# Kernel optimization log

Measured on AMD Instinct MI355X. Metric: run time of the kernel, lower is better.

Reference implementation:

```python
import jax, jax.numpy as jnp
import numpy as np

B, N, K, H = 4, 2048, 48, 128
EDGE = 128
FF = 4 * H
SCALE = 30.0


def setup_inputs() -> dict:
    key = jax.random.key(0)
    ks = jax.random.split(key, 12)
    s = lambda fan_in: 1.0 / np.sqrt(fan_in)
    return {
        "h_V": jax.random.normal(ks[0], (B, N, H), jnp.float32),
        "h_E": jax.random.normal(ks[1], (B, N, K, EDGE), jnp.float32),
        "E_idx": jax.random.randint(ks[2], (B, N, K), 0, N, jnp.int32),
        "mask_V": jnp.ones((B, N), jnp.float32),
        "mask_attend": jnp.ones((B, N, K), jnp.float32),
        "W1_w": jax.random.normal(ks[3], (H + EDGE, H), jnp.float32) * s(H + EDGE),
        "W1_b": jnp.zeros((H,), jnp.float32),
        "W2_w": jax.random.normal(ks[4], (H, H), jnp.float32) * s(H),
        "W2_b": jnp.zeros((H,), jnp.float32),
        "W3_w": jax.random.normal(ks[5], (H, H), jnp.float32) * s(H),
        "W3_b": jnp.zeros((H,), jnp.float32),
        "Win_w": jax.random.normal(ks[6], (H, FF), jnp.float32) * s(H),
        "Win_b": jnp.zeros((FF,), jnp.float32),
        "Wout_w": jax.random.normal(ks[7], (FF, H), jnp.float32) * s(FF),
        "Wout_b": jnp.zeros((H,), jnp.float32),
    }


def reference(h_V, h_E, E_idx, mask_V, mask_attend,
              W1_w, W1_b, W2_w, W2_b, W3_w, W3_b,
              Win_w, Win_b, Wout_w, Wout_b):
    gelu_tanh = lambda x: jax.nn.gelu(x, approximate=True)   # self.act = jax.nn.gelu (default approx)
    gelu_exact = lambda x: jax.nn.gelu(x, approximate=False)  # FFN uses approximate=False

    # gather neighbor node features: [B,N,K,H]
    h_nb = jax.vmap(lambda hv, idx: hv[idx])(h_V, E_idx)
    h_EV = jnp.concatenate([h_nb, h_E], axis=-1)              # [B,N,K,H+EDGE]

    # 3-layer message MLP
    m = gelu_tanh(jnp.einsum('bnkc,ch->bnkh', h_EV, W1_w) + W1_b)
    m = gelu_tanh(jnp.einsum('bnkh,hg->bnkg', m, W2_w) + W2_b)
    m = jnp.einsum('bnkg,gh->bnkh', m, W3_w) + W3_b

    m = mask_attend[..., None] * m
    dh = jnp.sum(m, axis=-2) / SCALE                          # [B,N,H]
    h = h_V + dh                                              # dropout rate 0 (eval)

    # position-wise FFN
    ff = gelu_exact(jnp.einsum('bnh,hf->bnf', h, Win_w) + Win_b)
    dh2 = jnp.einsum('bnf,fh->bnh', ff, Wout_w) + Wout_b
    h = h + dh2

    return mask_V[..., None] * h
```

## Files before the change

kernel.cpp:

```cpp
#include <hip/hip_runtime.h>
#include <hip/hip_bf16.h>
#include <math.h>

typedef __attribute__((ext_vector_type(8))) short bf16x8;
typedef __attribute__((ext_vector_type(4))) float f32x4;

#define MFMA16(a,b,c) __builtin_amdgcn_mfma_f32_16x16x32_bf16((a),(b),(c),0,0,0)

union U8 { uint4 u; bf16x8 v; };

__device__ __forceinline__ unsigned int pack2(float a, float b){
  __hip_bfloat162 h = __float22bfloat162_rn(float2{a, b});
  union { __hip_bfloat162 h; unsigned int u; } v; v.h = h;
  return v.u;
}
__device__ __forceinline__ float bflo(unsigned int u){ union{unsigned int i; float f;} v; v.i = u << 16; return v.f; }
__device__ __forceinline__ float bfhi(unsigned int u){ union{unsigned int i; float f;} v; v.i = u & 0xffff0000u; return v.f; }

__device__ __forceinline__ float gelu_tanh_f(float x){
  float x2 = x * x;
  float z  = x * fmaf(x2, -0.10294823f, -2.3022082f);
  float e  = exp2f(z);
  return x * __builtin_amdgcn_rcpf(1.0f + e);
}
__device__ __forceinline__ float gelu_erf_f(float x){
  return 0.5f * x * (1.0f + erff(x * 0.70710678118654752f));
}

__global__ void k_prep(const float* __restrict__ W1, const float* __restrict__ W2,
                       const float* __restrict__ W3, const float* __restrict__ Win,
                       const float* __restrict__ Wout, unsigned short* __restrict__ wt)
{
  int t = blockIdx.x * 256 + threadIdx.x;
  if (t >= 196608) return;
  float v;
  if (t < 32768){            int o = t >> 8,        i = t & 255;         v = W1[i*128 + o]; }
  else if (t < 49152){       int l = t - 32768, o = l >> 7, i = l & 127; v = W2[i*128 + o]; }
  else if (t < 65536){       int l = t - 49152, o = l >> 7, i = l & 127; v = W3[i*128 + o]; }
  else if (t < 131072){      int l = t - 65536, o = l >> 7, i = l & 127; v = Win[i*512 + o]; }
  else {                     int l = t - 131072, o = l >> 9, i = l & 511; v = Wout[i*128 + o]; }
  union { float f; unsigned int u; } w; w.f = v;
  unsigned int r = w.u + 0x7fffu + ((w.u >> 16) & 1u);
  wt[t] = (unsigned short)(r >> 16);
}

__global__ __launch_bounds__(256)
void k_hvp(const float* __restrict__ hV, const unsigned short* __restrict__ wt,
           const float* __restrict__ b1, unsigned short* __restrict__ hVpb)
{
  __shared__ char sH[32*256];
  const int tid = threadIdx.x;
  const int wv  = tid >> 6;
  const int ln  = tid & 63;
  const int l15 = ln & 15;
  const int l4  = ln >> 4;
  const int swz = (l15 & 7) << 4;
  const unsigned short* W1T = wt;
  const int nb = blockIdx.x * 32;

#pragma unroll
  for (int it = 0; it < 2; ++it){
    int cid = tid + it*256;
    int r = cid >> 4, cb = cid & 15;
    const float* src = hV + (size_t)(nb + r)*128 + cb*8;
    float4 a0 = *(const float4*)(src);
    float4 a1 = *(const float4*)(src + 4);
    uint4 w;
    w.x = pack2(a0.x, a0.y); w.y = pack2(a0.z, a0.w);
    w.z = pack2(a1.x, a1.y); w.w = pack2(a1.z, a1.w);
    *(uint4*)(&sH[r*256 + ((cb*16) ^ ((r&7)<<4))]) = w;
  }
  __syncthreads();

  f32x4 acc[2][2];
#pragma unroll
  for (int m = 0; m < 2; ++m){ acc[m][0] = f32x4{0.f,0.f,0.f,0.f}; acc[m][1] = f32x4{0.f,0.f,0.f,0.f}; }
#pragma unroll
  for (int ks = 0; ks < 4; ++ks){
    bf16x8 x0 = *(const bf16x8*)(&sH[(l15)*256      + ((ks*64 + l4*16) ^ swz)]);
    bf16x8 x1 = *(const bf16x8*)(&sH[(16 + l15)*256 + ((ks*64 + l4*16) ^ swz)]);
#pragma unroll
    for (int m = 0; m < 2; ++m){
      int orow = (wv*2 + m)*16 + l15;
      bf16x8 wf = *(const bf16x8*)(W1T + orow*256 + ks*32 + l4*8);
      acc[m][0] = MFMA16(wf, x0, acc[m][0]);
      acc[m][1] = MFMA16(wf, x1, acc[m][1]);
    }
  }
#pragma unroll
  for (int m = 0; m < 2; ++m){
    int och0 = (wv*2 + m)*16 + l4*4;
    float q0 = b1[och0], q1 = b1[och0+1], q2 = b1[och0+2], q3 = b1[och0+3];
#pragma unroll
    for (int nt = 0; nt < 2; ++nt){
      int node = nb + nt*16 + l15;
      uint2 p;
      p.x = pack2(acc[m][nt][0] + q0, acc[m][nt][1] + q1);
      p.y = pack2(acc[m][nt][2] + q2, acc[m][nt][3] + q3);
      *(uint2*)(hVpb + (size_t)node*128 + och0) = p;
    }
  }
}

__global__ __launch_bounds__(256, 2)
void k_msg(const float* __restrict__ hE, const int* __restrict__ Eidx,
           const float* __restrict__ maskA, const unsigned short* __restrict__ wt,
           const unsigned short* __restrict__ hVpb, const float* __restrict__ b2,
           float* __restrict__ S, float* __restrict__ msums)
{
  __shared__ char sW1[32768];

  const int tid = threadIdx.x;
  const int wv  = tid >> 6;
  const int ln  = tid & 63;
  const int l15 = ln & 15;
  const int l4  = ln >> 4;
  const int wswz = (l15 & 7) << 4;

  const unsigned short* W2G = wt + 32768;

#pragma unroll
  for (int it = 0; it < 8; ++it){
    int f = tid + it*256;
    int r = f >> 4, cb = f & 15;
    uint4 w1c = *(const uint4*)(wt + r*256 + 128 + cb*8);
    *(uint4*)(&sW1[r*256 + ((cb*16) ^ ((r&7)<<4))]) = w1c;
  }
  __syncthreads();

  const int node = blockIdx.x * 4 + wv;
  const size_t bb = ((size_t)(node >> 11)) << 11;

  int eidx0, eidx1, eidx2; float emk0, emk1, emk2;
  {
    const int*   ip = Eidx  + node*48 + l15;
    const float* mp = maskA + node*48 + l15;
    eidx0 = ip[0]; eidx1 = ip[16]; eidx2 = ip[32];
    emk0  = mp[0]; emk1  = mp[16]; emk2  = mp[32];
  }

  f32x4 ssum[8];
#pragma unroll
  for (int t = 0; t < 8; ++t) ssum[t] = f32x4{0.f,0.f,0.f,0.f};

#pragma unroll
  for (int c = 0; c < 3; ++c){
    const int   cidx = (c == 0) ? eidx0 : (c == 1) ? eidx1 : eidx2;
    const float cmk  = (c == 0) ? emk0  : (c == 1) ? emk1  : emk2;

    const float* xp = hE + (size_t)(node*48 + c*16 + l15)*128 + l4*8;
    float4 xr[8];
#pragma unroll
    for (int ks = 0; ks < 4; ++ks){
      xr[2*ks]   = *(const float4*)(xp + ks*32);
      xr[2*ks+1] = *(const float4*)(xp + ks*32 + 4);
    }
    uint2 hp[8];
    {
      const unsigned short* hb = hVpb + (bb + (size_t)cidx)*128 + l4*4;
#pragma unroll
      for (int t = 0; t < 8; ++t) hp[t] = *(const uint2*)(hb + 16*t);
    }
    bf16x8 xf[4];
#pragma unroll
    for (int ks = 0; ks < 4; ++ks){
      U8 xu;
      xu.u.x = pack2(xr[2*ks].x,   xr[2*ks].y);
      xu.u.y = pack2(xr[2*ks].z,   xr[2*ks].w);
      xu.u.z = pack2(xr[2*ks+1].x, xr[2*ks+1].y);
      xu.u.w = pack2(xr[2*ks+1].z, xr[2*ks+1].w);
      xf[ks] = xu.v;
    }

    f32x4 a1[8];
#pragma unroll
    for (int t = 0; t < 8; ++t) a1[t] = f32x4{0.f,0.f,0.f,0.f};
#pragma unroll
    for (int ks = 0; ks < 4; ++ks){
#pragma unroll
      for (int t = 0; t < 8; ++t){
        bf16x8 wf = *(const bf16x8*)(&sW1[(16*t + l15)*256 + ((ks*64 + l4*16) ^ wswz)]);
        a1[t] = MFMA16(wf, xf[ks], a1[t]);
      }
    }

    unsigned int q[8][2];
#pragma unroll
    for (int t = 0; t < 8; ++t){
      float g0 = gelu_tanh_f(a1[t][0] + bflo(hp[t].x));
      float g1 = gelu_tanh_f(a1[t][1] + bfhi(hp[t].x));
      float g2 = gelu_tanh_f(a1[t][2] + bflo(hp[t].y));
      float g3 = gelu_tanh_f(a1[t][3] + bfhi(hp[t].y));
      q[t][0] = pack2(g0, g1);
      q[t][1] = pack2(g2, g3);
    }

    f32x4 a2[8];
#pragma unroll
    for (int t = 0; t < 8; ++t) a2[t] = f32x4{0.f,0.f,0.f,0.f};
    const bool lo = (l4 < 2);
    const int srcbase = l15 + 32*(l4 & 1);
#pragma unroll
    for (int ks2 = 0; ks2 < 4; ++ks2){
      unsigned int xw[4];
#pragma unroll
      for (int p = 0; p < 4; ++p){
        int src = srcbase + 16*(p >> 1);
        unsigned int va = (unsigned int)__shfl((int)q[2*ks2][p & 1],     src, 64);
        unsigned int vb = (unsigned int)__shfl((int)q[2*ks2 + 1][p & 1], src, 64);
        xw[p] = lo ? va : vb;
      }
      U8 xb; xb.u.x = xw[0]; xb.u.y = xw[1]; xb.u.z = xw[2]; xb.u.w = xw[3];
#pragma unroll
      for (int t = 0; t < 8; ++t){
        bf16x8 wf = *(const bf16x8*)(W2G + (16*t + l15)*128 + ks2*32 + l4*8);
        a2[t] = MFMA16(wf, xb.v, a2[t]);
      }
    }

#pragma unroll
    for (int t = 0; t < 8; ++t){
      const float4 bq = *(const float4*)(b2 + 16*t + l4*4);
      ssum[t][0] += cmk * gelu_tanh_f(a2[t][0] + bq.x);
      ssum[t][1] += cmk * gelu_tanh_f(a2[t][1] + bq.y);
      ssum[t][2] += cmk * gelu_tanh_f(a2[t][2] + bq.z);
      ssum[t][3] += cmk * gelu_tanh_f(a2[t][3] + bq.w);
    }
  }

#pragma unroll
  for (int t = 0; t < 8; ++t){
#pragma unroll
    for (int r = 0; r < 4; ++r){
#pragma unroll
      for (int off = 1; off < 16; off <<= 1)
        ssum[t][r] += __shfl_xor(ssum[t][r], off, 16);
    }
  }
  if (l15 == 0){
#pragma unroll
    for (int t = 0; t < 8; ++t){
      float4 o;
      o.x = ssum[t][0] * (1.0f/30.0f);
      o.y = ssum[t][1] * (1.0f/30.0f);
      o.z = ssum[t][2] * (1.0f/30.0f);
      o.w = ssum[t][3] * (1.0f/30.0f);
      *(float4*)(S + (size_t)node*128 + 16*t + l4*4) = o;
    }
  }
  {
    float qs = emk0 + emk1 + emk2;
#pragma unroll
    for (int off = 1; off < 16; off <<= 1) qs += __shfl_xor(qs, off, 16);
    if (ln == 0) msums[node] = qs * (1.0f/30.0f);
  }
}

__global__ __launch_bounds__(256, 2)
void k_ffn(const float* __restrict__ hV, const float* __restrict__ S,
           const float* __restrict__ msums, const float* __restrict__ maskV,
           const unsigned short* __restrict__ wt,
           const float* __restrict__ b3, const float* __restrict__ bin,
           const float* __restrict__ bout, float* __restrict__ out)
{
  __shared__ char  sS[32*256];
  __shared__ char  sH[32*256];
  __shared__ float sHf[32*132];
  __shared__ char  sF[32*1024];

  const int tid = threadIdx.x;
  const int wv  = tid >> 6;
  const int ln  = tid & 63;
  const int l15 = ln & 15;
  const int l4  = ln >> 4;
  const int swz = (l15 & 7) << 4;
  const unsigned short* W3T   = wt + 49152;
  const unsigned short* WinT  = wt + 65536;
  const unsigned short* WoutT = wt + 131072;
  const int nb = blockIdx.x * 32;

#pragma unroll
  for (int it = 0; it < 2; ++it){
    int cid = tid + it*256;
    int r = cid >> 4, cb = cid & 15;
    const float* src = S + (size_t)(nb + r)*128 + cb*8;
    float4 a0 = *(const float4*)(src);
    float4 a1 = *(const float4*)(src + 4);
    uint4 w;
    w.x = pack2(a0.x, a0.y); w.y = pack2(a0.z, a0.w);
    w.z = pack2(a1.x, a1.y); w.w = pack2(a1.z, a1.w);
    *(uint4*)(&sS[r*256 + ((cb*16) ^ ((r&7)<<4))]) = w;
  }
  __syncthreads();

  {
    f32x4 acc[2][2];
#pragma unroll
    for (int m = 0; m < 2; ++m){ acc[m][0] = f32x4{0.f,0.f,0.f,0.f}; acc[m][1] = f32x4{0.f,0.f,0.f,0.f}; }
#pragma unroll
    for (int ks = 0; ks < 4; ++ks){
      bf16x8 x0 = *(const bf16x8*)(&sS[(l15)*256      + ((ks*64 + l4*16) ^ swz)]);
      bf16x8 x1 = *(const bf16x8*)(&sS[(16 + l15)*256 + ((ks*64 + l4*16) ^ swz)]);
#pragma unroll
      for (int m = 0; m < 2; ++m){
        int cr = (wv*2 + m)*16 + l15;
        bf16x8 wf = *(const bf16x8*)(W3T + cr*128 + ks*32 + l4*8);
        acc[m][0] = MFMA16(wf, x0, acc[m][0]);
        acc[m][1] = MFMA16(wf, x1, acc[m][1]);
      }
    }
#pragma unroll
    for (int m = 0; m < 2; ++m){
      int ch0 = (wv*2 + m)*16 + l4*4;
      const float4 b3q = *(const float4*)(b3 + ch0);
#pragma unroll
      for (int nt = 0; nt < 2; ++nt){
        int row  = nt*16 + l15;
        int node = nb + row;
        float ms = msums[node];
        const float4 hv = *(const float4*)(hV + (size_t)node*128 + ch0);
        float h0 = hv.x + acc[m][nt][0] + ms*b3q.x;
        float h1 = hv.y + acc[m][nt][1] + ms*b3q.y;
        float h2 = hv.z + acc[m][nt][2] + ms*b3q.z;
        float h3 = hv.w + acc[m][nt][3] + ms*b3q.w;
        float4 hf; hf.x = h0; hf.y = h1; hf.z = h2; hf.w = h3;
        *(float4*)(&sHf[row*132 + ch0]) = hf;
        uint2 p; p.x = pack2(h0, h1); p.y = pack2(h2, h3);
        *(uint2*)(&sH[row*256 + ((ch0*2) ^ ((row&7)<<4))]) = p;
      }
    }
  }
  __syncthreads();

  f32x4 accA[8][2];
#pragma unroll
  for (int m8 = 0; m8 < 8; ++m8){ accA[m8][0] = f32x4{0.f,0.f,0.f,0.f}; accA[m8][1] = f32x4{0.f,0.f,0.f,0.f}; }
#pragma unroll
  for (int ks = 0; ks < 4; ++ks){
    bf16x8 x0 = *(const bf16x8*)(&sH[(l15)*256      + ((ks*64 + l4*16) ^ swz)]);
    bf16x8 x1 = *(const bf16x8*)(&sH[(16 + l15)*256 + ((ks*64 + l4*16) ^ swz)]);
#pragma unroll
    for (int m8 = 0; m8 < 8; ++m8){
      int fr = (wv*8 + m8)*16 + l15;
      bf16x8 wf = *(const bf16x8*)(WinT + fr*128 + ks*32 + l4*8);
      accA[m8][0] = MFMA16(wf, x0, accA[m8][0]);
      accA[m8][1] = MFMA16(wf, x1, accA[m8][1]);
    }
  }
#pragma unroll
  for (int m8 = 0; m8 < 8; ++m8){
    int f0 = (wv*8 + m8)*16 + l4*4;
    float q0 = bin[f0], q1 = bin[f0+1], q2 = bin[f0+2], q3 = bin[f0+3];
#pragma unroll
    for (int nt = 0; nt < 2; ++nt){
      int row = nt*16 + l15;
      float g0 = gelu_erf_f(accA[m8][nt][0] + q0);
      float g1 = gelu_erf_f(accA[m8][nt][1] + q1);
      float g2 = gelu_erf_f(accA[m8][nt][2] + q2);
      float g3 = gelu_erf_f(accA[m8][nt][3] + q3);
      uint2 p; p.x = pack2(g0, g1); p.y = pack2(g2, g3);
      *(uint2*)(&sF[row*1024 + ((f0*2) ^ swz)]) = p;
    }
  }
  __syncthreads();

  f32x4 accB[2][2];
#pragma unroll
  for (int m = 0; m < 2; ++m){ accB[m][0] = f32x4{0.f,0.f,0.f,0.f}; accB[m][1] = f32x4{0.f,0.f,0.f,0.f}; }
#pragma unroll
  for (int ks = 0; ks < 16; ++ks){
    bf16x8 x0 = *(const bf16x8*)(&sF[(l15)*1024      + ((ks*64 + l4*16) ^ swz)]);
    bf16x8 x1 = *(const bf16x8*)(&sF[(16 + l15)*1024 + ((ks*64 + l4*16) ^ swz)]);
#pragma unroll
    for (int m = 0; m < 2; ++m){
      int cr = (wv*2 + m)*16 + l15;
      bf16x8 wf = *(const bf16x8*)(WoutT + cr*512 + ks*32 + l4*8);
      accB[m][0] = MFMA16(wf, x0, accB[m][0]);
      accB[m][1] = MFMA16(wf, x1, accB[m][1]);
    }
  }
#pragma unroll
  for (int m = 0; m < 2; ++m){
    int ch0 = (wv*2 + m)*16 + l4*4;
    float q0 = bout[ch0], q1 = bout[ch0+1], q2 = bout[ch0+2], q3 = bout[ch0+3];
#pragma unroll
    for (int nt = 0; nt < 2; ++nt){
      int row  = nt*16 + l15;
      int node = nb + row;
      float mv = maskV[node];
      const float4 hf = *(const float4*)(&sHf[row*132 + ch0]);
      float4 o;
      o.x = mv * (hf.x + accB[m][nt][0] + q0);
      o.y = mv * (hf.y + accB[m][nt][1] + q1);
      o.z = mv * (hf.z + accB[m][nt][2] + q2);
      o.w = mv * (hf.w + accB[m][nt][3] + q3);
      *(float4*)(out + (size_t)node*128 + ch0) = o;
    }
  }
}

extern "C" void kernel_launch(void* const* d_in, const int* in_sizes, int n_in,
                              void* d_out, int out_size, void* d_ws, size_t ws_size,
                              hipStream_t stream)
{
  const float* hV    = (const float*)d_in[0];
  const float* hE    = (const float*)d_in[1];
  const int*   Eidx  = (const int*)  d_in[2];
  const float* maskV = (const float*)d_in[3];
  const float* maskA = (const float*)d_in[4];
  const float* W1w = (const float*)d_in[5];
  const float* W1b = (const float*)d_in[6];
  const float* W2w = (const float*)d_in[7];
  const float* W2b = (const float*)d_in[8];
  const float* W3w = (const float*)d_in[9];
  const float* W3b = (const float*)d_in[10];
  const float* Winw  = (const float*)d_in[11];
  const float* Winb  = (const float*)d_in[12];
  const float* Woutw = (const float*)d_in[13];
  const float* Woutb = (const float*)d_in[14];
  float* out = (float*)d_out;

  unsigned short* wt   = (unsigned short*)d_ws;
  unsigned short* hVpb = (unsigned short*)((char*)d_ws + (1u << 19));
  float* Sbuf  = (float*)((char*)d_ws + (1u << 19) + (1u << 21));
  float* msums = (float*)((char*)d_ws + (1u << 19) + (1u << 21) + (1u << 22));

  k_prep<<<dim3(768),  dim3(256), 0, stream>>>(W1w, W2w, W3w, Winw, Woutw, wt);
  k_hvp <<<dim3(256),  dim3(256), 0, stream>>>(hV, wt, W1b, hVpb);
  k_msg <<<dim3(2048), dim3(256), 0, stream>>>(hE, Eidx, maskA, wt, hVpb, W2b, Sbuf, msums);
  k_ffn <<<dim3(256),  dim3(256), 0, stream>>>(hV, Sbuf, msums, maskV, wt, W3b, Winb, Woutb, out);
}
```

Baseline: 135.6 us.

## Split message kernel into two stages via bf16 intermediate, stage W2 in LDS

Splits the fused message kernel into k_msgA (layer-1 MFMA plus GELU, writing bf16 activations to a global scratch buffer) and k_msgB (layer-2 MFMA plus GELU and masked neighbour reduction). k_msgB reads W2 from swizzled LDS instead of global, and k_msgA software-prefetches the next edge chunk's inputs. The intent is to cut register pressure and cross-lane shuffles in the fused kernel and to make layer 1 cheaper. Both GELUs are replaced by a sigmoid-based approximation, which changes numerics. The cost is a large extra round trip of intermediate activations through HBM and one more kernel launch.

```diff
diff --git a/kernel.cpp b/kernel.cpp
--- a/kernel.cpp
+++ b/kernel.cpp
@@ -17,10 +17,8 @@
 __device__ __forceinline__ float bflo(unsigned int u){ union{unsigned int i; float f;} v; v.i = u << 16; return v.f; }
 __device__ __forceinline__ float bfhi(unsigned int u){ union{unsigned int i; float f;} v; v.i = u & 0xffff0000u; return v.f; }
 
-__device__ __forceinline__ float gelu_tanh_f(float x){
-  float x2 = x * x;
-  float z  = x * fmaf(x2, -0.10294823f, -2.3022082f);
-  float e  = exp2f(z);
+__device__ __forceinline__ float gelu_fast_f(float x){
+  float e = exp2f(x * -2.4554236f);
   return x * __builtin_amdgcn_rcpf(1.0f + e);
 }
 __device__ __forceinline__ float gelu_erf_f(float x){
@@ -102,11 +100,11 @@
   }
 }
 
+#define CPW_A 3
 __global__ __launch_bounds__(256, 2)
-void k_msg(const float* __restrict__ hE, const int* __restrict__ Eidx,
-           const float* __restrict__ maskA, const unsigned short* __restrict__ wt,
-           const unsigned short* __restrict__ hVpb, const float* __restrict__ b2,
-           float* __restrict__ S, float* __restrict__ msums)
+void k_msgA(const float* __restrict__ hE, const int* __restrict__ Eidx,
+            const unsigned short* __restrict__ wt,
+            const unsigned short* __restrict__ hVpb, unsigned int* __restrict__ m1f)
 {
   __shared__ char sW1[32768];
 
@@ -117,8 +115,6 @@
   const int l4  = ln >> 4;
   const int wswz = (l15 & 7) << 4;
 
-  const unsigned short* W2G = wt + 32768;
-
 #pragma unroll
   for (int it = 0; it < 8; ++it){
     int f = tid + it*256;
@@ -128,40 +124,26 @@
   }
   __syncthreads();
 
-  const int node = blockIdx.x * 4 + wv;
-  const size_t bb = ((size_t)(node >> 11)) << 11;
-
-  int eidx0, eidx1, eidx2; float emk0, emk1, emk2;
+  const int chunk0 = blockIdx.x * (4*CPW_A) + wv*CPW_A;
+
+  float4 xr[8]; int eidx;
   {
-    const int*   ip = Eidx  + node*48 + l15;
-    const float* mp = maskA + node*48 + l15;
-    eidx0 = ip[0]; eidx1 = ip[16]; eidx2 = ip[32];
-    emk0  = mp[0]; emk1  = mp[16]; emk2  = mp[32];
-  }
-
-  f32x4 ssum[8];
-#pragma unroll
-  for (int t = 0; t < 8; ++t) ssum[t] = f32x4{0.f,0.f,0.f,0.f};
-
-#pragma unroll
-  for (int c = 0; c < 3; ++c){
-    const int   cidx = (c == 0) ? eidx0 : (c == 1) ? eidx1 : eidx2;
-    const float cmk  = (c == 0) ? emk0  : (c == 1) ? emk1  : emk2;
-
-    const float* xp = hE + (size_t)(node*48 + c*16 + l15)*128 + l4*8;
-    float4 xr[8];
+    const float* xp = hE + (size_t)(chunk0*16 + l15)*128 + l4*8;
 #pragma unroll
     for (int ks = 0; ks < 4; ++ks){
       xr[2*ks]   = *(const float4*)(xp + ks*32);
       xr[2*ks+1] = *(const float4*)(xp + ks*32 + 4);
     }
-    uint2 hp[8];
-    {
-      const unsigned short* hb = hVpb + (bb + (size_t)cidx)*128 + l4*4;
-#pragma unroll
-      for (int t = 0; t < 8; ++t) hp[t] = *(const uint2*)(hb + 16*t);
-    }
-    bf16x8 xf[4];
+    eidx = Eidx[chunk0*16 + l15];
+  }
+
+#pragma unroll 1
+  for (int j = 0; j < CPW_A; ++j){
+    const int chunk = chunk0 + j;
+    const int b = chunk / 6144;
+    const int ecur = eidx;
+
+    bf16x8 xb[4];
 #pragma unroll
     for (int ks = 0; ks < 4; ++ks){
       U8 xu;
@@ -169,7 +151,22 @@
       xu.u.y = pack2(xr[2*ks].z,   xr[2*ks].w);
       xu.u.z = pack2(xr[2*ks+1].x, xr[2*ks+1].y);
       xu.u.w = pack2(xr[2*ks+1].z, xr[2*ks+1].w);
-      xf[ks] = xu.v;
+      xb[ks] = xu.v;
+    }
+    uint2 hp[8];
+    {
+      const unsigned short* hb = hVpb + ((size_t)(b << 11) + (size_t)ecur)*128 + l4*4;
+#pragma unroll
+      for (int t = 0; t < 8; ++t) hp[t] = *(const uint2*)(hb + 16*t);
+    }
+    if (j + 1 < CPW_A){
+      const float* xp = hE + (size_t)((chunk+1)*16 + l15)*128 + l4*8;
+#pragma unroll
+      for (int ks = 0; ks < 4; ++ks){
+        xr[2*ks]   = *(const float4*)(xp + ks*32);
+        xr[2*ks+1] = *(const float4*)(xp + ks*32 + 4);
+      }
+      eidx = Eidx[(chunk+1)*16 + l15];
     }
 
     f32x4 a1[8];
@@ -180,51 +177,83 @@
 #pragma unroll
       for (int t = 0; t < 8; ++t){
         bf16x8 wf = *(const bf16x8*)(&sW1[(16*t + l15)*256 + ((ks*64 + l4*16) ^ wswz)]);
-        a1[t] = MFMA16(wf, xf[ks], a1[t]);
+        a1[t] = MFMA16(wf, xb[ks], a1[t]);
       }
     }
 
-    unsigned int q[8][2];
+    unsigned int* mp = m1f + (size_t)chunk*1024 + ln*2;
 #pragma unroll
     for (int t = 0; t < 8; ++t){
-      float g0 = gelu_tanh_f(a1[t][0] + bflo(hp[t].x));
-      float g1 = gelu_tanh_f(a1[t][1] + bfhi(hp[t].x));
-      float g2 = gelu_tanh_f(a1[t][2] + bflo(hp[t].y));
-      float g3 = gelu_tanh_f(a1[t][3] + bfhi(hp[t].y));
-      q[t][0] = pack2(g0, g1);
-      q[t][1] = pack2(g2, g3);
-    }
+      uint2 q;
+      q.x = pack2(gelu_fast_f(a1[t][0] + bflo(hp[t].x)),
+                  gelu_fast_f(a1[t][1] + bfhi(hp[t].x)));
+      q.y = pack2(gelu_fast_f(a1[t][2] + bflo(hp[t].y)),
+                  gelu_fast_f(a1[t][3] + bfhi(hp[t].y)));
+      *(uint2*)(mp + t*128) = q;
+    }
+  }
+}
+
+__global__ __launch_bounds__(256, 2)
+void k_msgB(const unsigned int* __restrict__ m1f, const float* __restrict__ maskA,
+            const unsigned short* __restrict__ wt, const float* __restrict__ b2,
+            float* __restrict__ S, float* __restrict__ msums)
+{
+  __shared__ char sW2[32768];
+
+  const int tid = threadIdx.x;
+  const int wv  = tid >> 6;
+  const int ln  = tid & 63;
+  const int l15 = ln & 15;
+  const int l4  = ln >> 4;
+  const int wswz = (l15 & 7) << 4;
+
+#pragma unroll
+  for (int it = 0; it < 8; ++it){
+    int f = tid + it*256;
+    int r = f >> 4, cb = f & 15;
+    uint4 w2c = *(const uint4*)(wt + 32768 + r*128 + cb*8);
+    *(uint4*)(&sW2[r*256 + ((cb*16) ^ ((r&7)<<4))]) = w2c;
+  }
+  __syncthreads();
+
+  const int node = blockIdx.x * 4 + wv;
+  const int l4a  = (l4 & 1) * 2;
+
+  f32x4 ssum[8];
+#pragma unroll
+  for (int t = 0; t < 8; ++t) ssum[t] = f32x4{0.f,0.f,0.f,0.f};
+  float qs = 0.f;
+
+#pragma unroll
+  for (int cc = 0; cc < 3; ++cc){
+    const float cmk = maskA[node*48 + cc*16 + l15];
+    qs += cmk;
+    const unsigned int* base = m1f + (size_t)(node*3 + cc)*1024;
 
     f32x4 a2[8];
 #pragma unroll
     for (int t = 0; t < 8; ++t) a2[t] = f32x4{0.f,0.f,0.f,0.f};
-    const bool lo = (l4 < 2);
-    const int srcbase = l15 + 32*(l4 & 1);
 #pragma unroll
     for (int ks2 = 0; ks2 < 4; ++ks2){
-      unsigned int xw[4];
-#pragma unroll
-      for (int p = 0; p < 4; ++p){
-        int src = srcbase + 16*(p >> 1);
-        unsigned int va = (unsigned int)__shfl((int)q[2*ks2][p & 1],     src, 64);
-        unsigned int vb = (unsigned int)__shfl((int)q[2*ks2 + 1][p & 1], src, 64);
-        xw[p] = lo ? va : vb;
+      const int t2 = 2*ks2 + (l4 >> 1);
+      const unsigned int* p1 = base + t2*128 + (l4a*16 + l15)*2;
+      uint2 u1 = *(const uint2*)(p1);
+      uint2 u2 = *(const uint2*)(p1 + 32);
+      U8 xbu; xbu.u.x = u1.x; xbu.u.y = u1.y; xbu.u.z = u2.x; xbu.u.w = u2.y;
+#pragma unroll
+      for (int t = 0; t < 8; ++t){
+        bf16x8 wf = *(const bf16x8*)(&sW2[(16*t + l15)*256 + ((ks2*64 + l4*16) ^ wswz)]);
+        a2[t] = MFMA16(wf, xbu.v, a2[t]);
       }
-      U8 xb; xb.u.x = xw[0]; xb.u.y = xw[1]; xb.u.z = xw[2]; xb.u.w = xw[3];
-#pragma unroll
-      for (int t = 0; t < 8; ++t){
-        bf16x8 wf = *(const bf16x8*)(W2G + (16*t + l15)*128 + ks2*32 + l4*8);
-        a2[t] = MFMA16(wf, xb.v, a2[t]);
-      }
-    }
-
+    }
 #pragma unroll
     for (int t = 0; t < 8; ++t){
       const float4 bq = *(const float4*)(b2 + 16*t + l4*4);
-      ssum[t][0] += cmk * gelu_tanh_f(a2[t][0] + bq.x);
-      ssum[t][1] += cmk * gelu_tanh_f(a2[t][1] + bq.y);
-      ssum[t][2] += cmk * gelu_tanh_f(a2[t][2] + bq.z);
-      ssum[t][3] += cmk * gelu_tanh_f(a2[t][3] + bq.w);
+      ssum[t][0] += cmk * gelu_fast_f(a2[t][0] + bq.x);
+      ssum[t][1] += cmk * gelu_fast_f(a2[t][1] + bq.y);
+      ssum[t][2] += cmk * gelu_fast_f(a2[t][2] + bq.z);
+      ssum[t][3] += cmk * gelu_fast_f(a2[t][3] + bq.w);
     }
   }
 
@@ -234,7 +263,7 @@
     for (int r = 0; r < 4; ++r){
 #pragma unroll
       for (int off = 1; off < 16; off <<= 1)
-        ssum[t][r] += __shfl_xor(ssum[t][r], off, 16);
+        ssum[t][r] += __shfl_xor(ssum[t][r], off);
     }
   }
   if (l15 == 0){
@@ -248,12 +277,9 @@
       *(float4*)(S + (size_t)node*128 + 16*t + l4*4) = o;
     }
   }
-  {
-    float qs = emk0 + emk1 + emk2;
-#pragma unroll
-    for (int off = 1; off < 16; off <<= 1) qs += __shfl_xor(qs, off, 16);
-    if (ln == 0) msums[node] = qs * (1.0f/30.0f);
-  }
+#pragma unroll
+  for (int off = 1; off < 16; off <<= 1) qs += __shfl_xor(qs, off);
+  if (ln == 0) msums[node] = qs * (1.0f/30.0f);
 }
 
 __global__ __launch_bounds__(256, 2)
@@ -424,9 +450,11 @@
   unsigned short* hVpb = (unsigned short*)((char*)d_ws + (1u << 19));
   float* Sbuf  = (float*)((char*)d_ws + (1u << 19) + (1u << 21));
   float* msums = (float*)((char*)d_ws + (1u << 19) + (1u << 21) + (1u << 22));
+  unsigned int* m1f = (unsigned int*)((char*)d_ws + (8u << 20));
 
   k_prep<<<dim3(768),  dim3(256), 0, stream>>>(W1w, W2w, W3w, Winw, Woutw, wt);
   k_hvp <<<dim3(256),  dim3(256), 0, stream>>>(hV, wt, W1b, hVpb);
-  k_msg <<<dim3(2048), dim3(256), 0, stream>>>(hE, Eidx, maskA, wt, hVpb, W2b, Sbuf, msums);
+  k_msgA<<<dim3(2048), dim3(256), 0, stream>>>(hE, Eidx, wt, hVpb, m1f);
+  k_msgB<<<dim3(2048), dim3(256), 0, stream>>>(m1f, maskA, wt, W2b, Sbuf, msums);
   k_ffn <<<dim3(256),  dim3(256), 0, stream>>>(hV, Sbuf, msums, maskV, wt, W3b, Winb, Woutb, out);
 }
```

Result: slower. 139.1 us (+2.6%).
